# Kernel optimization log

Measured on AMD Instinct MI355X. Metric: run time of the kernel, lower is better.

## Reference

```python
import jax, jax.numpy as jnp
import numpy as np

B, S, H, I, RH, P, K, NH = 4, 1024, 1024, 4096, 256, 16, 4, 16
TEMP = 1.0


def setup_inputs() -> dict:
    key = jax.random.key(0)
    ks = jax.random.split(key, 10)
    g = lambda k, shape: (jax.random.normal(k, shape, jnp.float32) * 0.02)
    return {
        "hidden_states": jax.random.normal(ks[0], (B, S, H), jnp.float32),
        "ln1_w": jnp.ones((H,), jnp.float32),
        "ln1_b": jnp.zeros((H,), jnp.float32),
        "Wqkv": g(ks[1], (3 * H, H)),
        "bqkv": jnp.zeros((3 * H,), jnp.float32),
        "Wo": g(ks[2], (H, H)),
        "bo": jnp.zeros((H,), jnp.float32),
        "ln2_w": jnp.ones((H,), jnp.float32),
        "ln2_b": jnp.zeros((H,), jnp.float32),
        "Wr1": g(ks[3], (RH, H)),
        "br1": jnp.zeros((RH,), jnp.float32),
        "Wr2": g(ks[4], (P, RH)),
        "br2": jnp.zeros((P,), jnp.float32),
        "W1": g(ks[5], (I, H)),
        "b1": jnp.zeros((I,), jnp.float32),
        "W2": g(ks[6], (H, I)),
        "b2": jnp.zeros((H,), jnp.float32),
    }


def _layernorm(x, w, b, eps=1e-5):
    m = x.mean(-1, keepdims=True)
    v = jnp.mean((x - m) ** 2, axis=-1, keepdims=True)
    return (x - m) * jax.lax.rsqrt(v + eps) * w + b


def _forward(hidden_states, ln1_w, ln1_b, Wqkv, bqkv, Wo, bo,
             ln2_w, ln2_b, Wr1, br1, Wr2, br2, W1, b1, W2, b2):
    Dh = H // NH
    # --- attention sub-block (GPT-2 style causal self-attention) ---
    x = _layernorm(hidden_states, ln1_w, ln1_b)
    qkv = x @ Wqkv.T + bqkv                                  # [B,S,3H]
    q, k, v = jnp.split(qkv, 3, axis=-1)
    split = lambda t: t.reshape(B, S, NH, Dh).transpose(0, 2, 1, 3)  # [B,NH,S,Dh]
    q, k, v = split(q), split(k), split(v)
    scores = jnp.einsum('bhqd,bhkd->bhqk', q, k) * (1.0 / np.float32(np.sqrt(Dh)))
    causal = jnp.tril(jnp.ones((S, S), bool))
    scores = jnp.where(causal, scores, jnp.float32(-1e9))
    attn = jax.nn.softmax(scores, axis=-1)
    ctx = jnp.einsum('bhqk,bhkd->bhqd', attn, v)
    ctx = ctx.transpose(0, 2, 1, 3).reshape(B, S, H)
    h = hidden_states + ctx @ Wo.T + bo                      # residual 1

    # --- routed MLP sub-block ---
    x2 = _layernorm(h, ln2_w, ln2_b)
    # router MLP (eval mode: no dropout)
    r = jax.nn.relu(x2 @ Wr1.T + br1) @ Wr2.T + br2          # [B,S,P]
    probs = jax.nn.softmax(r / TEMP, axis=-1)
    top_vals, top_idx = jax.lax.top_k(probs, K)              # [B,S,K]
    # scatter top-k probs back to pathway axis, then renormalize
    sel = jnp.sum(jax.nn.one_hot(top_idx, P, dtype=probs.dtype) * top_vals[..., None], axis=-2)  # [B,S,P]
    w = sel / (sel.sum(-1, keepdims=True) + 1e-8)

    # block-diagonal pathway MLP: pathway p uses contiguous slices of W1/W2
    Hp, Ip = H // P, I // P
    pidx = jnp.arange(P)
    W1b = W1.reshape(P, Ip, P, Hp)[pidx, :, pidx, :]         # [P,Ip,Hp]
    b1b = b1.reshape(P, Ip)
    W2b = W2.reshape(P, Hp, P, Ip)[pidx, :, pidx, :]         # [P,Hp,Ip]
    b2b = b2.reshape(P, Hp)
    hb = x2.reshape(B, S, P, Hp)
    inter = jax.nn.gelu(jnp.einsum('bsph,pih->bspi', hb, W1b) + b1b)
    po = jnp.einsum('bspi,phi->bsph', inter, W2b) + b2b       # [B,S,P,Hp]
    mlp_out = (po * w[..., None]).reshape(B, S, H)
    return h + mlp_out


def reference(hidden_states, ln1_w, ln1_b, Wqkv, bqkv, Wo, bo,
              ln2_w, ln2_b, Wr1, br1, Wr2, br2, W1, b1, W2, b2):
    return _forward(hidden_states, ln1_w, ln1_b, Wqkv, bqkv, Wo, bo,
                    ln2_w, ln2_b, Wr1, br1, Wr2, br2, W1, b1, W2, b2)
```

## Files before the change

kernel.cpp:

```cpp
#include <hip/hip_runtime.h>


#define USH unsigned short

typedef __attribute__((ext_vector_type(8))) short s16x8;
typedef __attribute__((ext_vector_type(4))) float f32x4;

__device__ __forceinline__ float bf2f(USH u) {
    union { unsigned int i; float f; } x; x.i = ((unsigned int)u) << 16; return x.f;
}
__device__ __forceinline__ USH f2bf(float f) {
    unsigned int x = __float_as_uint(f);
    unsigned int r = (x + 0x7fffu + ((x >> 16) & 1u)) >> 16;
    return (USH)r;
}
__device__ __forceinline__ const USH* pick(const void* raw, const USH* ar, bool bf16in) {
    return bf16in ? (const USH*)raw : ar;
}

__device__ __forceinline__ void async16(const USH* g, USH* lds_base) {
    __builtin_amdgcn_global_load_lds((const __attribute__((address_space(1))) unsigned int*)g,
                                     (__attribute__((address_space(3))) unsigned int*)lds_base,
                                     16, 0, 0);
}

struct CvtArgs {
    const void* src[17];
    unsigned off[18];
};

__global__ __launch_bounds__(256) void convert_kernel(CvtArgs a, USH* __restrict__ arena,
                                                      const unsigned* __restrict__ det)
{
    if (*det != 0x3F800000u) return;
    int s = blockIdx.y + 1;
    unsigned n4 = (a.off[s + 1] - a.off[s]) >> 2;
    ushort4* dst = (ushort4*)(arena + a.off[s]);
    const float4* sf = (const float4*)a.src[s];
    for (unsigned i = blockIdx.x * 256u + threadIdx.x; i < n4; i += gridDim.x * 256u) {
        float4 f = sf[i];
        ushort4 o;
        o.x = f2bf(f.x); o.y = f2bf(f.y); o.z = f2bf(f.z); o.w = f2bf(f.w);
        dst[i] = o;
    }
}

__global__ __launch_bounds__(256) void ln_kernel(const void* __restrict__ in,
                                                 const unsigned* __restrict__ det,
                                                 const void* __restrict__ gwr, const USH* __restrict__ gwa,
                                                 const void* __restrict__ gbr, const USH* __restrict__ gba,
                                                 const unsigned* __restrict__ wdet,
                                                 USH* __restrict__ out)
{
    bool bf16w = (*wdet != 0x3F800000u);
    const USH* gw = pick(gwr, gwa, bf16w);
    const USH* gb = pick(gbr, gba, bf16w);
    int row = blockIdx.x, tid = threadIdx.x;
    bool bf16in = det && (*det != 0x3F800000u);
    float v0, v1, v2, v3;
    if (bf16in) {
        const USH* r = (const USH*)in + (size_t)row * 1024 + tid * 4;
        ushort4 u = *(const ushort4*)r;
        v0 = bf2f(u.x); v1 = bf2f(u.y); v2 = bf2f(u.z); v3 = bf2f(u.w);
    } else {
        const float* r = (const float*)in + (size_t)row * 1024 + tid * 4;
        float4 f = *(const float4*)r;
        v0 = f.x; v1 = f.y; v2 = f.z; v3 = f.w;
    }
    float s = v0 + v1 + v2 + v3;
    float q = v0*v0 + v1*v1 + v2*v2 + v3*v3;
    #pragma unroll
    for (int o = 32; o >= 1; o >>= 1) { s += __shfl_xor(s, o); q += __shfl_xor(q, o); }
    __shared__ float rs[4], rq[4];
    int wid = tid >> 6;
    if ((tid & 63) == 0) { rs[wid] = s; rq[wid] = q; }
    __syncthreads();
    float S = rs[0] + rs[1] + rs[2] + rs[3];
    float Q = rq[0] + rq[1] + rq[2] + rq[3];
    float mean = S * (1.0f / 1024.0f);
    float var  = Q * (1.0f / 1024.0f) - mean * mean;
    float rstd = rsqrtf(var + 1e-5f);
    int c = tid * 4;
    ushort4 wv = *(const ushort4*)(gw + c);
    ushort4 bv = *(const ushort4*)(gb + c);
    ushort4 o4;
    o4.x = f2bf((v0 - mean) * rstd * bf2f(wv.x) + bf2f(bv.x));
    o4.y = f2bf((v1 - mean) * rstd * bf2f(wv.y) + bf2f(bv.y));
    o4.z = f2bf((v2 - mean) * rstd * bf2f(wv.z) + bf2f(bv.z));
    o4.w = f2bf((v3 - mean) * rstd * bf2f(wv.w) + bf2f(bv.w));
    *(ushort4*)(out + (size_t)row * 1024 + c) = o4;
}

template<int RT, int CT>
__global__ __launch_bounds__(256) void gemm_t(
    const USH* __restrict__ A,
    const void* __restrict__ Wraw, const USH* __restrict__ Warena,
    const void* __restrict__ braw, const USH* __restrict__ barena,
    void* __restrict__ Cout, const void* __restrict__ resid,
    int M, int N, int K, int mode, const unsigned* __restrict__ det)
{
    constexpr int BM = 32 * RT, BN = 32 * CT;
    constexpr int NA8 = BM / 8, NC8 = (BM + BN) / 8, NPW = NC8 / 4;
    bool bf16in = (*det != 0x3F800000u);
    const USH* W    = pick(Wraw, Warena, bf16in);
    const USH* bias = pick(braw, barena, bf16in);
    __shared__ __align__(16) USH As[BM * 64];
    __shared__ __align__(16) USH Bs[BN * 64];
    int tid = threadIdx.x;
    int w = tid >> 6, lane = tid & 63, l15 = lane & 15, quad = lane >> 4;
    int wm = (w & 1) * 16 * RT, wn = (w >> 1) * 16 * CT;
    int m0 = blockIdx.x * BM, n0 = blockIdx.y * BN;
    int lr8 = lane >> 3, g = (lane & 7) ^ lr8;
    int sw = l15 & 7;

    const USH* cp[NPW]; USH* lp[NPW];
    #pragma unroll
    for (int i = 0; i < NPW; ++i) {
        int c = w + 4 * i;
        if (c < NA8) { cp[i] = A + (size_t)(m0 + c * 8 + lr8) * K + g * 8;            lp[i] = &As[c * 512]; }
        else         { cp[i] = W + (size_t)(n0 + (c - NA8) * 8 + lr8) * K + g * 8;    lp[i] = &Bs[(c - NA8) * 512]; }
    }
    f32x4 acc[RT][CT] = {};
    for (int k0 = 0; k0 < K; k0 += 64) {
        __syncthreads();
        #pragma unroll
        for (int i = 0; i < NPW; ++i) { async16(cp[i], lp[i]); cp[i] += 64; }
        __syncthreads();
        s16x8 af[RT][2], bfr[CT][2];
        #pragma unroll
        for (int i = 0; i < RT; ++i) {
            int r = wm + 16*i + l15;
            af[i][0] = *(const s16x8*)&As[r * 64 + ((quad       ^ sw) * 8)];
            af[i][1] = *(const s16x8*)&As[r * 64 + (((quad + 4) ^ sw) * 8)];
        }
        #pragma unroll
        for (int j = 0; j < CT; ++j) {
            int r = wn + 16*j + l15;
            bfr[j][0] = *(const s16x8*)&Bs[r * 64 + ((quad       ^ sw) * 8)];
            bfr[j][1] = *(const s16x8*)&Bs[r * 64 + (((quad + 4) ^ sw) * 8)];
        }
        #pragma unroll
        for (int i = 0; i < RT; ++i)
            #pragma unroll
            for (int j = 0; j < CT; ++j) {
                acc[i][j] = __builtin_amdgcn_mfma_f32_16x16x32_bf16(af[i][0], bfr[j][0], acc[i][j], 0, 0, 0);
                acc[i][j] = __builtin_amdgcn_mfma_f32_16x16x32_bf16(af[i][1], bfr[j][1], acc[i][j], 0, 0, 0);
            }
    }
    bool rf32 = !bf16in;
    float bv[CT];
    #pragma unroll
    for (int j = 0; j < CT; ++j) bv[j] = bf2f(bias[n0 + wn + 16*j + l15]);
    #pragma unroll
    for (int i = 0; i < RT; ++i) {
        int mrow = m0 + wm + 16*i + quad * 4;
        #pragma unroll
        for (int j = 0; j < CT; ++j) {
            int n = n0 + wn + 16*j + l15;
            #pragma unroll
            for (int r = 0; r < 4; ++r) {
                int m = mrow + r;
                float val = acc[i][j][r] + bv[j];
                if (mode == 3) val = fmaxf(val, 0.0f);
                if (mode == 2) {
                    size_t idx = (size_t)m * N + n;
                    val += rf32 ? ((const float*)resid)[idx] : bf2f(((const USH*)resid)[idx]);
                }
                if (mode == 1) {
                    int which = n >> 10, head = (n >> 6) & 15, d = n & 63;
                    int b = m >> 10, sdx = m & 1023;
                    ((USH*)Cout)[(((size_t)(which * 64 + b * 16 + head)) * 1024 + sdx) * 64 + d] = f2bf(val);
                } else {
                    ((float*)Cout)[(size_t)m * N + n] = val;
                }
            }
        }
    }
}

__global__ __launch_bounds__(256) void attn_mfma(const USH* __restrict__ qkv,
                                                 USH* __restrict__ ctx)
{
    int bh = blockIdx.x;
    int qb = (gridDim.y - 1) - blockIdx.y;
    int q0 = qb * 64;
    int tid = threadIdx.x, w = tid >> 6, lane = tid & 63, l15 = lane & 15, quad = lane >> 4;
    __shared__ __align__(16) USH Kt[64][72];
    __shared__ __align__(16) USH Vt[80][72];
    __shared__ __align__(16) USH Pb[4][16][72];
    const USH* Qb = qkv + (size_t)bh * 65536;
    const USH* Kb = qkv + (size_t)(64 + bh) * 65536;
    const USH* Vb = qkv + (size_t)(128 + bh) * 65536;
    s16x8 qf[2];
    {
        const USH* qp = Qb + (size_t)(q0 + 16*w + l15) * 64 + quad * 8;
        qf[0] = *(const s16x8*)qp;
        qf[1] = *(const s16x8*)(qp + 32);
    }
    for (int i = tid; i < 16 * 72; i += 256) (&Vt[64][0])[i] = 0x3F80;
    f32x4 oacc[4] = {};
    f32x4 lacc = {};
    int sr = tid & 63, scb = tid >> 6;
    int rowb = 16*w + quad * 4;
    for (int kt = 0; kt <= qb; ++kt) {
        int k0 = kt << 6;
        __syncthreads();
        {
            const USH* kg = Kb + (size_t)(k0 + sr) * 64 + scb * 16;
            uint4 k0v = *(const uint4*)kg;
            uint4 k1v = *(const uint4*)(kg + 8);
            *(uint4*)&Kt[sr][scb * 16]     = k0v;
            *(uint4*)&Kt[sr][scb * 16 + 8] = k1v;
            const USH* vg = Vb + (size_t)(k0 + sr) * 64 + scb * 16;
            uint4 v0v = *(const uint4*)vg;
            uint4 v1v = *(const uint4*)(vg + 8);
            USH tmp[16];
            *(uint4*)tmp       = v0v;
            *(uint4*)(tmp + 8) = v1v;
            #pragma unroll
            for (int i = 0; i < 16; ++i) Vt[scb * 16 + i][sr] = tmp[i];
        }
        __syncthreads();
        f32x4 sacc[4] = {};
        #pragma unroll
        for (int t = 0; t < 4; ++t) {
            s16x8 kf0 = *(const s16x8*)&Kt[16*t + l15][quad * 8];
            s16x8 kf1 = *(const s16x8*)&Kt[16*t + l15][32 + quad * 8];
            sacc[t] = __builtin_amdgcn_mfma_f32_16x16x32_bf16(qf[0], kf0, sacc[t], 0, 0, 0);
            sacc[t] = __builtin_amdgcn_mfma_f32_16x16x32_bf16(qf[1], kf1, sacc[t], 0, 0, 0);
        }
        bool diag = (kt == qb);
        #pragma unroll
        for (int t = 0; t < 4; ++t)
            #pragma unroll
            for (int r = 0; r < 4; ++r) {
                bool masked = diag && (16*t + l15 > rowb + r);
                float pv = masked ? 0.0f : __expf(sacc[t][r] * 0.125f);
                Pb[w][quad*4 + r][16*t + l15] = f2bf(pv);
            }
        s16x8 pf0 = *(const s16x8*)&Pb[w][l15][quad * 8];
        s16x8 pf1 = *(const s16x8*)&Pb[w][l15][32 + quad * 8];
        #pragma unroll
        for (int t = 0; t < 4; ++t) {
            s16x8 vf0 = *(const s16x8*)&Vt[16*t + l15][quad * 8];
            s16x8 vf1 = *(const s16x8*)&Vt[16*t + l15][32 + quad * 8];
            oacc[t] = __builtin_amdgcn_mfma_f32_16x16x32_bf16(pf0, vf0, oacc[t], 0, 0, 0);
            oacc[t] = __builtin_amdgcn_mfma_f32_16x16x32_bf16(pf1, vf1, oacc[t], 0, 0, 0);
        }
        s16x8 of0 = *(const s16x8*)&Vt[64 + l15][quad * 8];
        s16x8 of1 = *(const s16x8*)&Vt[64 + l15][32 + quad * 8];
        lacc = __builtin_amdgcn_mfma_f32_16x16x32_bf16(pf0, of0, lacc, 0, 0, 0);
        lacc = __builtin_amdgcn_mfma_f32_16x16x32_bf16(pf1, of1, lacc, 0, 0, 0);
    }
    int b = bh >> 4, hh = bh & 15;
    float inv[4];
    #pragma unroll
    for (int r = 0; r < 4; ++r) inv[r] = 1.0f / lacc[r];
    #pragma unroll
    for (int t = 0; t < 4; ++t)
        #pragma unroll
        for (int r = 0; r < 4; ++r) {
            int q = q0 + 16*w + quad * 4 + r;
            int d = 16*t + l15;
            ctx[((size_t)(b * 1024 + q)) * 1024 + hh * 64 + d] = f2bf(oacc[t][r] * inv[r]);
        }
}

__global__ __launch_bounds__(64) void router_kernel(const float* __restrict__ r1,
                                                    const void* __restrict__ Wr2raw, const USH* __restrict__ Wr2a,
                                                    const void* __restrict__ br2raw, const USH* __restrict__ br2a,
                                                    const unsigned* __restrict__ det,
                                                    float* __restrict__ wout)
{
    bool bf16in = (*det != 0x3F800000u);
    const USH* Wr2 = pick(Wr2raw, Wr2a, bf16in);
    const USH* br2 = pick(br2raw, br2a, bf16in);
    int tok = blockIdx.x, lane = threadIdx.x;
    int p = lane & 15, c = lane >> 4;
    const float* row = r1 + (size_t)tok * 256;
    const USH* wr = Wr2 + p * 256 + c * 64;
    float s = 0.0f;
    #pragma unroll
    for (int i = 0; i < 64; i += 4) {
        ushort4 u = *(const ushort4*)(wr + i);
        s = fmaf(bf2f(u.x), row[c*64 + i + 0], s);
        s = fmaf(bf2f(u.y), row[c*64 + i + 1], s);
        s = fmaf(bf2f(u.z), row[c*64 + i + 2], s);
        s = fmaf(bf2f(u.w), row[c*64 + i + 3], s);
    }
    s += __shfl_xor(s, 16);
    s += __shfl_xor(s, 32);
    s += bf2f(br2[p]);
    float mx = s;
    #pragma unroll
    for (int o = 8; o >= 1; o >>= 1) mx = fmaxf(mx, __shfl_xor(mx, o));
    float e = __expf(s - mx);
    float sum = e;
    #pragma unroll
    for (int o = 8; o >= 1; o >>= 1) sum += __shfl_xor(sum, o);
    float prob = e / sum;
    int rank = 0;
    int base = lane & 48;
    #pragma unroll
    for (int j = 0; j < 16; ++j) {
        float pj = __shfl(prob, base + j);
        rank += (pj > prob) || (pj == prob && j < p);
    }
    float sel = (rank < 4) ? prob : 0.0f;
    float ssum = sel;
    #pragma unroll
    for (int o = 8; o >= 1; o >>= 1) ssum += __shfl_xor(ssum, o);
    float wv = sel / (ssum + 1e-8f);
    if (lane < 16) wout[(size_t)tok * 16 + lane] = wv;
}

__global__ __launch_bounds__(256) void pw_fused(
    const USH* __restrict__ x2,
    const void* __restrict__ W1raw, const USH* __restrict__ W1a,
    const void* __restrict__ b1raw, const USH* __restrict__ b1a,
    const void* __restrict__ W2raw, const USH* __restrict__ W2a,
    const void* __restrict__ b2raw, const USH* __restrict__ b2a,
    const float* __restrict__ hbuf, const float* __restrict__ wbuf,
    void* __restrict__ out, const unsigned* __restrict__ det)
{
    bool bf16in = (*det != 0x3F800000u);
    const USH* W1 = pick(W1raw, W1a, bf16in);
    const USH* b1 = pick(b1raw, b1a, bf16in);
    const USH* W2 = pick(W2raw, W2a, bf16in);
    const USH* b2 = pick(b2raw, b2a, bf16in);
    int p = blockIdx.y;
    int m0 = blockIdx.x * 64;
    __shared__ __align__(16) USH lds[32768];
    USH* As  = lds;
    USH* Bs1 = lds + 4096;
    USH* Is  = lds;
    USH* Bs2 = lds + 16384;
    int tid = threadIdx.x;
    int w = tid >> 6, lane = tid & 63, l15 = lane & 15, quad = lane >> 4;
    int lr8 = lane >> 3, g = (lane & 7) ^ lr8;
    int sw = l15 & 7;

    #pragma unroll
    for (int i = 0; i < 10; ++i) {
        int c = w + 4 * i;
        if (c < 8) async16(x2 + (size_t)(m0 + c * 8 + lr8) * 1024 + p * 64 + g * 8, &As[c * 512]);
        else       async16(W1 + (size_t)(p * 256 + (c - 8) * 8 + lr8) * 1024 + p * 64 + g * 8, &Bs1[(c - 8) * 512]);
    }
    __syncthreads();

    int wmA = (w & 1) * 32, wnA = (w >> 1) * 128;
    f32x4 accA[2][8] = {};
    {
        s16x8 af[2][2];
        #pragma unroll
        for (int i = 0; i < 2; ++i) {
            int r = wmA + 16*i + l15;
            af[i][0] = *(const s16x8*)&As[r * 64 + ((quad       ^ sw) * 8)];
            af[i][1] = *(const s16x8*)&As[r * 64 + (((quad + 4) ^ sw) * 8)];
        }
        #pragma unroll
        for (int j = 0; j < 8; ++j) {
            int r = wnA + 16*j + l15;
            s16x8 b0 = *(const s16x8*)&Bs1[r * 64 + ((quad       ^ sw) * 8)];
            s16x8 b1f = *(const s16x8*)&Bs1[r * 64 + (((quad + 4) ^ sw) * 8)];
            #pragma unroll
            for (int i = 0; i < 2; ++i) {
                accA[i][j] = __builtin_amdgcn_mfma_f32_16x16x32_bf16(af[i][0], b0,  accA[i][j], 0, 0, 0);
                accA[i][j] = __builtin_amdgcn_mfma_f32_16x16x32_bf16(af[i][1], b1f, accA[i][j], 0, 0, 0);
            }
        }
    }
    __syncthreads();

    #pragma unroll
    for (int ks = 0; ks < 4; ++ks)
        #pragma unroll
        for (int i = 0; i < 2; ++i) {
            int c = w + 4 * i;
            async16(W2 + (size_t)(p * 64 + c * 8 + lr8) * 4096 + p * 256 + ks * 64 + g * 8,
                    &Bs2[ks * 4096 + c * 512]);
        }

    #pragma unroll
    for (int j = 0; j < 8; ++j) {
        int n1 = wnA + 16*j + l15;
        float bias1 = bf2f(b1[p * 256 + n1]);
        int slab = n1 >> 6, cs = (n1 >> 3) & 7, e = n1 & 7;
        #pragma unroll
        for (int i = 0; i < 2; ++i) {
            int mb = wmA + 16*i + quad * 4;
            #pragma unroll
            for (int r = 0; r < 4; ++r) {
                int m = mb + r;
                float s = accA[i][j][r] + bias1;
                float u = 0.7978845608028654f * (s + 0.044715f * s * s * s);
                float eu = __expf(2.0f * u);
                float gl = s * (1.0f - 1.0f / (eu + 1.0f));
                Is[slab * 4096 + m * 64 + ((cs ^ (m & 7)) * 8) + e] = f2bf(gl);
            }
        }
    }
    __syncthreads();

    int wmB = (w & 1) * 32, wnB = (w >> 1) * 32;
    f32x4 accB[2][2] = {};
    #pragma unroll
    for (int ks = 0; ks < 4; ++ks) {
        s16x8 af[2][2], bfr[2][2];
        #pragma unroll
        for (int i = 0; i < 2; ++i) {
            int r = wmB + 16*i + l15;
            af[i][0] = *(const s16x8*)&Is[ks * 4096 + r * 64 + ((quad       ^ sw) * 8)];
            af[i][1] = *(const s16x8*)&Is[ks * 4096 + r * 64 + (((quad + 4) ^ sw) * 8)];
        }
        #pragma unroll
        for (int j = 0; j < 2; ++j) {
            int r = wnB + 16*j + l15;
            bfr[j][0] = *(const s16x8*)&Bs2[ks * 4096 + r * 64 + ((quad       ^ sw) * 8)];
            bfr[j][1] = *(const s16x8*)&Bs2[ks * 4096 + r * 64 + (((quad + 4) ^ sw) * 8)];
        }
        #pragma unroll
        for (int i = 0; i < 2; ++i)
            #pragma unroll
            for (int j = 0; j < 2; ++j) {
                accB[i][j] = __builtin_amdgcn_mfma_f32_16x16x32_bf16(af[i][0], bfr[j][0], accB[i][j], 0, 0, 0);
                accB[i][j] = __builtin_amdgcn_mfma_f32_16x16x32_bf16(af[i][1], bfr[j][1], accB[i][j], 0, 0, 0);
            }
    }

    bool f32out = !bf16in;
    #pragma unroll
    for (int i = 0; i < 2; ++i) {
        int tok0 = m0 + wmB + 16*i + quad * 4;
        float wp[4];
        #pragma unroll
        for (int r = 0; r < 4; ++r) wp[r] = wbuf[(size_t)(tok0 + r) * 16 + p];
        #pragma unroll
        for (int j = 0; j < 2; ++j) {
            int hl = wnB + 16*j + l15;
            int hcol = p * 64 + hl;
            float bias2 = bf2f(b2[p * 64 + hl]);
            #pragma unroll
            for (int r = 0; r < 4; ++r) {
                size_t o = (size_t)(tok0 + r) * 1024 + hcol;
                float val = hbuf[o] + (accB[i][j][r] + bias2) * wp[r];
                if (f32out) ((float*)out)[o] = val;
                else        ((USH*)out)[o]   = f2bf(val);
            }
        }
    }
}

extern "C" void kernel_launch(void* const* d_in, const int* in_sizes, int n_in,
                              void* d_out, int out_size, void* d_ws, size_t ws_size,
                              hipStream_t stream) {
    (void)n_in; (void)out_size; (void)ws_size;
    const unsigned* det = (const unsigned*)d_in[1];

    CvtArgs ca;
    unsigned off = 0;
    for (int i = 0; i < 17; ++i) { ca.src[i] = d_in[i]; ca.off[i] = off; off += (unsigned)in_sizes[i]; }
    ca.off[17] = off;

    USH* arena = (USH*)d_ws;
    const USH* ln1w_a = arena + ca.off[1];
    const USH* ln1b_a = arena + ca.off[2];
    const USH* Wqkv_a = arena + ca.off[3];
    const USH* bqkv_a = arena + ca.off[4];
    const USH* Wo_a   = arena + ca.off[5];
    const USH* bo_a   = arena + ca.off[6];
    const USH* ln2w_a = arena + ca.off[7];
    const USH* ln2b_a = arena + ca.off[8];
    const USH* Wr1_a  = arena + ca.off[9];
    const USH* br1_a  = arena + ca.off[10];
    const USH* Wr2_a  = arena + ca.off[11];
    const USH* br2_a  = arena + ca.off[12];
    const USH* W1_a   = arena + ca.off[13];
    const USH* b1_a   = arena + ca.off[14];
    const USH* W2_a   = arena + ca.off[15];
    const USH* b2_a   = arena + ca.off[16];

    size_t arenaB = ((size_t)off * 2 + 255) & ~(size_t)255;
    char* base = (char*)d_ws;
    USH*   x     = (USH*)(base + arenaB);
    USH*   qkvt  = (USH*)(base + arenaB + 8388608);
    float* h     = (float*)(base + arenaB + 8388608 + 25165824);
    USH*   x2    = (USH*)(base + arenaB + 8388608 + 25165824 + 16777216);
    float* r1    = (float*)qkvt;
    float* wbuf  = (float*)(base + arenaB + 8388608 + 25165824 + 16777216 + 8388608);
    USH*   ctx   = x;

    convert_kernel<<<dim3(256, 16), 256, 0, stream>>>(ca, arena, det);
    ln_kernel<<<4096, 256, 0, stream>>>(d_in[0], det, d_in[1], ln1w_a, d_in[2], ln1b_a, det, x);
    gemm_t<4,4><<<dim3(32, 24), 256, 0, stream>>>(x, d_in[3], Wqkv_a, d_in[4], bqkv_a, qkvt, nullptr, 4096, 3072, 1024, 1, det);
    attn_mfma<<<dim3(64, 16), 256, 0, stream>>>(qkvt, ctx);
    gemm_t<2,4><<<dim3(64, 8), 256, 0, stream>>>(ctx, d_in[5], Wo_a, d_in[6], bo_a, h, d_in[0], 4096, 1024, 1024, 2, det);
    ln_kernel<<<4096, 256, 0, stream>>>(h, nullptr, d_in[7], ln2w_a, d_in[8], ln2b_a, det, x2);
    gemm_t<1,2><<<dim3(128, 4), 256, 0, stream>>>(x2, d_in[9], Wr1_a, d_in[10], br1_a, r1, nullptr, 4096, 256, 1024, 3, det);
    router_kernel<<<4096, 64, 0, stream>>>(r1, d_in[11], Wr2_a, d_in[12], br2_a, det, wbuf);
    pw_fused<<<dim3(64, 16), 256, 0, stream>>>(x2, d_in[13], W1_a, d_in[14], b1_a,
                                               d_in[15], W2_a, d_in[16], b2_a,
                                               h, wbuf, d_out, det);
}
```

Before: 285.0 us.

## Double-buffer GEMM LDS tiles and convert only diagonal W1/W2 blocks

The GEMM now keeps two LDS buffers and issues the next k-tile's async global-to-LDS loads before computing on the current tile. Explicit vmcnt waits and barriers replace the two syncthreads per iteration, so load latency can overlap with MFMA work. Separately, the fp32-to-bf16 conversion of W1 and W2 now touches only the block-diagonal pathway slices the MLP actually uses, which cuts conversion traffic. Doubling LDS may lower occupancy, and the hand-placed waitcnt and barrier logic must stay correct.

After: 289.7 us. About the same (+1.7%).

```diff
diff --git a/kernel.cpp b/kernel.cpp
--- a/kernel.cpp
+++ b/kernel.cpp
@@ -34,6 +34,18 @@
 {
     if (*det != 0x3F800000u) return;
     int s = blockIdx.y + 1;
+    if (s == 13 || s == 15) {
+        unsigned i = blockIdx.x * 256u + threadIdx.x;
+        unsigned p = i >> 12, rem = i & 4095u;
+        size_t e;
+        if (s == 13) { unsigned row = rem >> 4, c4 = rem & 15u; e = (size_t)(p * 256 + row) * 1024 + p * 64  + c4 * 4; }
+        else         { unsigned row = rem >> 6, c4 = rem & 63u; e = (size_t)(p * 64  + row) * 4096 + p * 256 + c4 * 4; }
+        float4 f = *(const float4*)((const float*)a.src[s] + e);
+        ushort4 o;
+        o.x = f2bf(f.x); o.y = f2bf(f.y); o.z = f2bf(f.z); o.w = f2bf(f.w);
+        *(ushort4*)(arena + a.off[s] + e) = o;
+        return;
+    }
     unsigned n4 = (a.off[s + 1] - a.off[s]) >> 2;
     ushort4* dst = (ushort4*)(arena + a.off[s]);
     const float4* sf = (const float4*)a.src[s];
@@ -104,8 +116,8 @@
     bool bf16in = (*det != 0x3F800000u);
     const USH* W    = pick(Wraw, Warena, bf16in);
     const USH* bias = pick(braw, barena, bf16in);
-    __shared__ __align__(16) USH As[BM * 64];
-    __shared__ __align__(16) USH Bs[BN * 64];
+    __shared__ __align__(16) USH As[2 * BM * 64];
+    __shared__ __align__(16) USH Bs[2 * BN * 64];
     int tid = threadIdx.x;
     int w = tid >> 6, lane = tid & 63, l15 = lane & 15, quad = lane >> 4;
     int wm = (w & 1) * 16 * RT, wn = (w >> 1) * 16 * CT;
@@ -113,32 +125,46 @@
     int lr8 = lane >> 3, g = (lane & 7) ^ lr8;
     int sw = l15 & 7;
 
-    const USH* cp[NPW]; USH* lp[NPW];
+    const USH* cp[NPW]; USH* lp[NPW]; int ls[NPW];
     #pragma unroll
     for (int i = 0; i < NPW; ++i) {
         int c = w + 4 * i;
-        if (c < NA8) { cp[i] = A + (size_t)(m0 + c * 8 + lr8) * K + g * 8;            lp[i] = &As[c * 512]; }
-        else         { cp[i] = W + (size_t)(n0 + (c - NA8) * 8 + lr8) * K + g * 8;    lp[i] = &Bs[(c - NA8) * 512]; }
-    }
+        if (c < NA8) { cp[i] = A + (size_t)(m0 + c * 8 + lr8) * K + g * 8;            lp[i] = &As[c * 512];            ls[i] = BM * 64; }
+        else         { cp[i] = W + (size_t)(n0 + (c - NA8) * 8 + lr8) * K + g * 8;    lp[i] = &Bs[(c - NA8) * 512];    ls[i] = BN * 64; }
+    }
+    int NT = K >> 6;
+    #pragma unroll
+    for (int i = 0; i < NPW; ++i) { async16(cp[i], lp[i]); cp[i] += 64; }
+
     f32x4 acc[RT][CT] = {};
-    for (int k0 = 0; k0 < K; k0 += 64) {
-        __syncthreads();
-        #pragma unroll
-        for (int i = 0; i < NPW; ++i) { async16(cp[i], lp[i]); cp[i] += 64; }
-        __syncthreads();
+    for (int t = 0; t < NT; ++t) {
+        int cur = t & 1;
+        if (t + 1 < NT) {
+            #pragma unroll
+            for (int i = 0; i < NPW; ++i) { async16(cp[i], lp[i] + (cur ? 0 : ls[i])); cp[i] += 64; }
+            asm volatile("s_waitcnt vmcnt(%0)" :: "n"(NPW) : "memory");
+        } else {
+            asm volatile("s_waitcnt vmcnt(0)" ::: "memory");
+        }
+        __builtin_amdgcn_s_barrier();
+        const USH* Ab = As + cur * (BM * 64);
+        const USH* Bb = Bs + cur * (BN * 64);
         s16x8 af[RT][2], bfr[CT][2];
         #pragma unroll
         for (int i = 0; i < RT; ++i) {
             int r = wm + 16*i + l15;
-            af[i][0] = *(const s16x8*)&As[r * 64 + ((quad       ^ sw) * 8)];
-            af[i][1] = *(const s16x8*)&As[r * 64 + (((quad + 4) ^ sw) * 8)];
+            af[i][0] = *(const s16x8*)&Ab[r * 64 + ((quad       ^ sw) * 8)];
+            af[i][1] = *(const s16x8*)&Ab[r * 64 + (((quad + 4) ^ sw) * 8)];
         }
         #pragma unroll
         for (int j = 0; j < CT; ++j) {
             int r = wn + 16*j + l15;
-            bfr[j][0] = *(const s16x8*)&Bs[r * 64 + ((quad       ^ sw) * 8)];
-            bfr[j][1] = *(const s16x8*)&Bs[r * 64 + (((quad + 4) ^ sw) * 8)];
-        }
+            bfr[j][0] = *(const s16x8*)&Bb[r * 64 + ((quad       ^ sw) * 8)];
+            bfr[j][1] = *(const s16x8*)&Bb[r * 64 + (((quad + 4) ^ sw) * 8)];
+        }
+        asm volatile("s_waitcnt lgkmcnt(0)" ::: "memory");
+        __builtin_amdgcn_sched_barrier(0);
+        __builtin_amdgcn_s_barrier();
         #pragma unroll
         for (int i = 0; i < RT; ++i)
             #pragma unroll
```

## Double attention query tile per block and convert only diagonal blocks of W1/W2

Applied to the files above, without the earlier changes.

The attention kernel now gives each block 128 query rows (32 per wave) instead of 64. Each K/V tile loaded into LDS is reused across twice as many queries, and the grid shrinks to 8 query blocks. The causal mask now uses absolute indices over the last two key tiles. Separately, the fp32-to-bf16 conversion of W1 and W2 writes only the block-diagonal pathway slices the MLP reads, skipping the off-diagonal weights. The trade-offs are fewer blocks for load balancing, more registers per wave, and some wasted work on masked tiles.

Result: no change. 286.9 us (+0.7%).

```diff
diff --git a/kernel.cpp b/kernel.cpp
--- a/kernel.cpp
+++ b/kernel.cpp
@@ -34,6 +34,18 @@
 {
     if (*det != 0x3F800000u) return;
     int s = blockIdx.y + 1;
+    if (s == 13 || s == 15) {
+        unsigned i = blockIdx.x * 256u + threadIdx.x;
+        unsigned p = i >> 12, rem = i & 4095u;
+        size_t e;
+        if (s == 13) { unsigned row = rem >> 4, c4 = rem & 15u; e = (size_t)(p * 256 + row) * 1024 + p * 64  + c4 * 4; }
+        else         { unsigned row = rem >> 6, c4 = rem & 63u; e = (size_t)(p * 64  + row) * 4096 + p * 256 + c4 * 4; }
+        float4 f = *(const float4*)((const float*)a.src[s] + e);
+        ushort4 o;
+        o.x = f2bf(f.x); o.y = f2bf(f.y); o.z = f2bf(f.z); o.w = f2bf(f.w);
+        *(ushort4*)(arena + a.off[s] + e) = o;
+        return;
+    }
     unsigned n4 = (a.off[s + 1] - a.off[s]) >> 2;
     ushort4* dst = (ushort4*)(arena + a.off[s]);
     const float4* sf = (const float4*)a.src[s];
@@ -183,26 +195,27 @@
 {
     int bh = blockIdx.x;
     int qb = (gridDim.y - 1) - blockIdx.y;
-    int q0 = qb * 64;
+    int q0 = qb * 128;
     int tid = threadIdx.x, w = tid >> 6, lane = tid & 63, l15 = lane & 15, quad = lane >> 4;
     __shared__ __align__(16) USH Kt[64][72];
     __shared__ __align__(16) USH Vt[80][72];
-    __shared__ __align__(16) USH Pb[4][16][72];
+    __shared__ __align__(16) USH Pb[4][32][72];
     const USH* Qb = qkv + (size_t)bh * 65536;
     const USH* Kb = qkv + (size_t)(64 + bh) * 65536;
     const USH* Vb = qkv + (size_t)(128 + bh) * 65536;
-    s16x8 qf[2];
-    {
-        const USH* qp = Qb + (size_t)(q0 + 16*w + l15) * 64 + quad * 8;
-        qf[0] = *(const s16x8*)qp;
-        qf[1] = *(const s16x8*)(qp + 32);
+    s16x8 qf[2][2];
+    #pragma unroll
+    for (int i = 0; i < 2; ++i) {
+        const USH* qp = Qb + (size_t)(q0 + 32*w + 16*i + l15) * 64 + quad * 8;
+        qf[i][0] = *(const s16x8*)qp;
+        qf[i][1] = *(const s16x8*)(qp + 32);
     }
     for (int i = tid; i < 16 * 72; i += 256) (&Vt[64][0])[i] = 0x3F80;
-    f32x4 oacc[4] = {};
-    f32x4 lacc = {};
+    f32x4 oacc[2][4] = {};
+    f32x4 lacc[2] = {};
     int sr = tid & 63, scb = tid >> 6;
-    int rowb = 16*w + quad * 4;
-    for (int kt = 0; kt <= qb; ++kt) {
+    int ktmax = 2 * qb + 1;
+    for (int kt = 0; kt <= ktmax; ++kt) {
         int k0 = kt << 6;
         __syncthreads();
         {
@@ -221,49 +234,71 @@
             for (int i = 0; i < 16; ++i) Vt[scb * 16 + i][sr] = tmp[i];
         }
         __syncthreads();
-        f32x4 sacc[4] = {};
+        f32x4 sacc[2][4] = {};
         #pragma unroll
         for (int t = 0; t < 4; ++t) {
             s16x8 kf0 = *(const s16x8*)&Kt[16*t + l15][quad * 8];
             s16x8 kf1 = *(const s16x8*)&Kt[16*t + l15][32 + quad * 8];
-            sacc[t] = __builtin_amdgcn_mfma_f32_16x16x32_bf16(qf[0], kf0, sacc[t], 0, 0, 0);
-            sacc[t] = __builtin_amdgcn_mfma_f32_16x16x32_bf16(qf[1], kf1, sacc[t], 0, 0, 0);
-        }
-        bool diag = (kt == qb);
-        #pragma unroll
-        for (int t = 0; t < 4; ++t)
-            #pragma unroll
-            for (int r = 0; r < 4; ++r) {
-                bool masked = diag && (16*t + l15 > rowb + r);
-                float pv = masked ? 0.0f : __expf(sacc[t][r] * 0.125f);
-                Pb[w][quad*4 + r][16*t + l15] = f2bf(pv);
-            }
-        s16x8 pf0 = *(const s16x8*)&Pb[w][l15][quad * 8];
-        s16x8 pf1 = *(const s16x8*)&Pb[w][l15][32 + quad * 8];
+            #pragma unroll
+            for (int i = 0; i < 2; ++i) {
+                sacc[i][t] = __builtin_amdgcn_mfma_f32_16x16x32_bf16(qf[i][0], kf0, sacc[i][t], 0, 0, 0);
+                sacc[i][t] = __builtin_amdgcn_mfma_f32_16x16x32_bf16(qf[i][1], kf1, sacc[i][t], 0, 0, 0);
+            }
+        }
+        bool diag = (kt >= 2 * qb);
+        #pragma unroll
+        for (int i = 0; i < 2; ++i) {
+            int rowb = q0 + 32*w + 16*i + quad * 4;
+            #pragma unroll
+            for (int t = 0; t < 4; ++t) {
+                int kabs = k0 + 16*t + l15;
+                #pragma unroll
+                for (int r = 0; r < 4; ++r) {
+                    bool masked = diag && (kabs > rowb + r);
+                    float pv = masked ? 0.0f : __expf(sacc[i][t][r] * 0.125f);
+                    Pb[w][16*i + quad*4 + r][16*t + l15] = f2bf(pv);
+                }
+            }
+        }
+        s16x8 pf0[2], pf1[2];
+        #pragma unroll
+        for (int i = 0; i < 2; ++i) {
+            pf0[i] = *(const s16x8*)&Pb[w][16*i + l15][quad * 8];
+            pf1[i] = *(const s16x8*)&Pb[w][16*i + l15][32 + quad * 8];
+        }
         #pragma unroll
         for (int t = 0; t < 4; ++t) {
             s16x8 vf0 = *(const s16x8*)&Vt[16*t + l15][quad * 8];
             s16x8 vf1 = *(const s16x8*)&Vt[16*t + l15][32 + quad * 8];
-            oacc[t] = __builtin_amdgcn_mfma_f32_16x16x32_bf16(pf0, vf0, oacc[t], 0, 0, 0);
-            oacc[t] = __builtin_amdgcn_mfma_f32_16x16x32_bf16(pf1, vf1, oacc[t], 0, 0, 0);
+            #pragma unroll
+            for (int i = 0; i < 2; ++i) {
+                oacc[i][t] = __builtin_amdgcn_mfma_f32_16x16x32_bf16(pf0[i], vf0, oacc[i][t], 0, 0, 0);
+                oacc[i][t] = __builtin_amdgcn_mfma_f32_16x16x32_bf16(pf1[i], vf1, oacc[i][t], 0, 0, 0);
+            }
         }
         s16x8 of0 = *(const s16x8*)&Vt[64 + l15][quad * 8];
         s16x8 of1 = *(const s16x8*)&Vt[64 + l15][32 + quad * 8];
-        lacc = __builtin_amdgcn_mfma_f32_16x16x32_bf16(pf0, of0, lacc, 0, 0, 0);
-        lacc = __builtin_amdgcn_mfma_f32_16x16x32_bf16(pf1, of1, lacc, 0, 0, 0);
+        #pragma unroll
+        for (int i = 0; i < 2; ++i) {
+            lacc[i] = __builtin_amdgcn_mfma_f32_16x16x32_bf16(pf0[i], of0, lacc[i], 0, 0, 0);
+            lacc[i] = __builtin_amdgcn_mfma_f32_16x16x32_bf16(pf1[i], of1, lacc[i], 0, 0, 0);
+        }
     }
     int b = bh >> 4, hh = bh & 15;
-    float inv[4];
-    #pragma unroll
-    for (int r = 0; r < 4; ++r) inv[r] = 1.0f / lacc[r];
-    #pragma unroll
-    for (int t = 0; t < 4; ++t)
-        #pragma unroll
-        for (int r = 0; r < 4; ++r) {
-            int q = q0 + 16*w + quad * 4 + r;
-            int d = 16*t + l15;
-            ctx[((size_t)(b * 1024 + q)) * 1024 + hh * 64 + d] = f2bf(oacc[t][r] * inv[r]);
-        }
+    #pragma unroll
+    for (int i = 0; i < 2; ++i) {
+        float inv[4];
+        #pragma unroll
+        for (int r = 0; r < 4; ++r) inv[r] = 1.0f / lacc[i][r];
+        #pragma unroll
+        for (int t = 0; t < 4; ++t)
+            #pragma unroll
+            for (int r = 0; r < 4; ++r) {
+                int q = q0 + 32*w + 16*i + quad * 4 + r;
+                int d = 16*t + l15;
+                ctx[((size_t)(b * 1024 + q)) * 1024 + hh * 64 + d] = f2bf(oacc[i][t][r] * inv[r]);
+            }
+    }
 }
 
 __global__ __launch_bounds__(64) void router_kernel(const float* __restrict__ r1,
@@ -493,7 +528,7 @@
     convert_kernel<<<dim3(256, 16), 256, 0, stream>>>(ca, arena, det);
     ln_kernel<<<4096, 256, 0, stream>>>(d_in[0], det, d_in[1], ln1w_a, d_in[2], ln1b_a, det, x);
     gemm_t<4,4><<<dim3(32, 24), 256, 0, stream>>>(x, d_in[3], Wqkv_a, d_in[4], bqkv_a, qkvt, nullptr, 4096, 3072, 1024, 1, det);
-    attn_mfma<<<dim3(64, 16), 256, 0, stream>>>(qkvt, ctx);
+    attn_mfma<<<dim3(64, 8), 256, 0, stream>>>(qkvt, ctx);
     gemm_t<2,4><<<dim3(64, 8), 256, 0, stream>>>(ctx, d_in[5], Wo_a, d_in[6], bo_a, h, d_in[0], 4096, 1024, 1024, 2, det);
     ln_kernel<<<4096, 256, 0, stream>>>(h, nullptr, d_in[7], ln2w_a, d_in[8], ln2b_a, det, x2);
     gemm_t<1,2><<<dim3(128, 4), 256, 0, stream>>>(x2, d_in[9], Wr1_a, d_in[10], br1_a, r1, nullptr, 4096, 256, 1024, 3, det);
```

## Remap block IDs for XCD-local L2 reuse and convert only diagonal pathway weights

Applied to the files above, without the earlier changes.

Remaps the linear block ID in the gemm, attention and pathway kernels so that blocks sharing the same tiles or heads land on the same XCD (id&7 round-robin), aiming for better L2 locality on MI355X. The convert kernel now converts only the block-diagonal slices of W1 and W2 for the fp32 input path, skipping the off-diagonal weights that are never read. The remapping assumes the grid size is divisible by 8 and hardcodes a 1024-block grid for attention and pathway, which could break with other shapes.

Result: slower. 294.7 us (+3.4%).

```diff
diff --git a/kernel.cpp b/kernel.cpp
--- a/kernel.cpp
+++ b/kernel.cpp
@@ -34,6 +34,18 @@
 {
     if (*det != 0x3F800000u) return;
     int s = blockIdx.y + 1;
+    if (s == 13 || s == 15) {
+        unsigned i = blockIdx.x * 256u + threadIdx.x;
+        unsigned p = i >> 12, rem = i & 4095u;
+        size_t e;
+        if (s == 13) { unsigned row = rem >> 4, c4 = rem & 15u; e = (size_t)(p * 256 + row) * 1024 + p * 64  + c4 * 4; }
+        else         { unsigned row = rem >> 6, c4 = rem & 63u; e = (size_t)(p * 64  + row) * 4096 + p * 256 + c4 * 4; }
+        float4 f = *(const float4*)((const float*)a.src[s] + e);
+        ushort4 o;
+        o.x = f2bf(f.x); o.y = f2bf(f.y); o.z = f2bf(f.z); o.w = f2bf(f.w);
+        *(ushort4*)(arena + a.off[s] + e) = o;
+        return;
+    }
     unsigned n4 = (a.off[s + 1] - a.off[s]) >> 2;
     ushort4* dst = (ushort4*)(arena + a.off[s]);
     const float4* sf = (const float4*)a.src[s];
@@ -109,7 +121,11 @@
     int tid = threadIdx.x;
     int w = tid >> 6, lane = tid & 63, l15 = lane & 15, quad = lane >> 4;
     int wm = (w & 1) * 16 * RT, wn = (w >> 1) * 16 * CT;
-    int m0 = blockIdx.x * BM, n0 = blockIdx.y * BN;
+    int id  = blockIdx.x + blockIdx.y * gridDim.x;
+    int per = (gridDim.x * gridDim.y) >> 3;
+    int nid = (id & 7) * per + (id >> 3);
+    int mt  = nid / gridDim.y, nt = nid - mt * gridDim.y;
+    int m0 = mt * BM, n0 = nt * BN;
     int lr8 = lane >> 3, g = (lane & 7) ^ lr8;
     int sw = l15 & 7;
 
@@ -181,8 +197,10 @@
 __global__ __launch_bounds__(256) void attn_mfma(const USH* __restrict__ qkv,
                                                  USH* __restrict__ ctx)
 {
-    int bh = blockIdx.x;
-    int qb = (gridDim.y - 1) - blockIdx.y;
+    int id  = blockIdx.x + blockIdx.y * gridDim.x;
+    int nid = (id & 7) * 128 + (id >> 3);
+    int bh = nid >> 4;
+    int qb = 15 - (nid & 15);
     int q0 = qb * 64;
     int tid = threadIdx.x, w = tid >> 6, lane = tid & 63, l15 = lane & 15, quad = lane >> 4;
     __shared__ __align__(16) USH Kt[64][72];
@@ -328,8 +346,10 @@
     const USH* b1 = pick(b1raw, b1a, bf16in);
     const USH* W2 = pick(W2raw, W2a, bf16in);
     const USH* b2 = pick(b2raw, b2a, bf16in);
-    int p = blockIdx.y;
-    int m0 = blockIdx.x * 64;
+    int id  = blockIdx.x + blockIdx.y * gridDim.x;
+    int nid = (id & 7) * 128 + (id >> 3);
+    int p  = nid >> 6;
+    int m0 = (nid & 63) * 64;
     __shared__ __align__(16) USH lds[32768];
     USH* As  = lds;
     USH* Bs1 = lds + 4096;
```
